# Performance work log

Hardware: AMD Instinct MI355X
Metric: run time of the kernel (lower is better)

## Reference

```python
import jax, jax.numpy as jnp
import numpy as np

N, B, T, H, M, DM, K = 256, 32, 128, 64, 8, 32, 3
IN_DIM = 1
OUT_DIM = 1
DEC_H = H + DM  # 96


def _p(key, shape):
    return jax.random.normal(key, shape, jnp.float32) / np.sqrt(shape[0]).astype(np.float32)


def setup_inputs() -> dict:
    key = jax.random.key(0)
    ks = jax.random.split(key, 10)
    gdi = 2 * K * (IN_DIM + H)      # 390
    ddi = 2 * K * (OUT_DIM + DEC_H)  # 582
    return {
        'x': jax.random.normal(ks[0], (B, T, N, IN_DIM), jnp.float32),
        'Memory': _p(ks[1], (M, DM)),
        'Wq': _p(ks[2], (H, DM)),
        'We1': _p(ks[3], (N, M)),
        'We2': _p(ks[4], (N, M)),
        'enc_gate_w': _p(ks[5], (gdi, 2 * H)), 'enc_gate_b': jnp.zeros((2 * H,), jnp.float32),
        'enc_upd_w': _p(ks[6], (gdi, H)), 'enc_upd_b': jnp.zeros((H,), jnp.float32),
        'dec_gate_w': _p(ks[7], (ddi, 2 * DEC_H)), 'dec_gate_b': jnp.zeros((2 * DEC_H,), jnp.float32),
        'dec_upd_w': _p(ks[8], (ddi, DEC_H)), 'dec_upd_b': jnp.zeros((DEC_H,), jnp.float32),
        'proj_w': _p(ks[9], (DEC_H, OUT_DIM)), 'proj_b': jnp.zeros((OUT_DIM,), jnp.float32),
    }


def _cheb(s):
    # Chebyshev polynomials T_0..T_{K-1} of support s: [I, s, 2 s T_{k-1} - T_{k-2}]
    polys = [jnp.eye(N, dtype=s.dtype), s]
    for _ in range(2, K):
        polys.append(2.0 * s @ polys[-1] - polys[-2])
    return polys


def _scaled_lap(e1, e2, gkey):
    # cosine-similarity graph -> straight-through gumbel hard selection -> scaled Laplacian
    norm = jnp.linalg.norm(e1, axis=1, keepdims=True) @ jnp.linalg.norm(e2, axis=1, keepdims=True).T
    g = (e1 @ e2.T) / (norm + 1e-6)
    g = (g + 1.0) / 2.0
    logits = jnp.stack([g, 1.0 - g], axis=-1)               # (N,N,2)
    y_soft = logits + jax.random.gumbel(gkey, logits.shape, logits.dtype)  # tau=1 (note: source skips softmax)
    y_hard = jax.nn.one_hot(jnp.argmax(y_soft, axis=-1), 2, dtype=logits.dtype)
    adj = (y_hard - jax.lax.stop_gradient(y_soft) + y_soft)[:, :, 0]
    eye = jnp.eye(N, dtype=adj.dtype)
    adj = adj * (1.0 - eye)                                  # zero diagonal
    d = jnp.sum(adj, axis=1)
    L = jnp.diag(d) - adj
    lam = L.max() - L.min()
    return 2.0 * L / lam - eye


def _gconv(x, S, w, b):
    # S: (2K,N,N) stacked cheb supports; x: (B,N,C)
    xg = jnp.einsum('knm,bmc->bnkc', S, x)
    xg = xg.reshape(xg.shape[0], xg.shape[1], -1)            # (B,N,2K*C), support-major like torch cat
    return xg @ w + b


def _cell(x, state, S, gw, gb, uw, ub, hid):
    zr = jax.nn.sigmoid(_gconv(jnp.concatenate([x, state], -1), S, gw, gb))
    z, r = zr[..., :hid], zr[..., hid:]
    hc = jnp.tanh(_gconv(jnp.concatenate([x, z * state], -1), S, uw, ub))
    return r * state + (1.0 - r) * hc


def reference(x, Memory, Wq, We1, We2, enc_gate_w, enc_gate_b, enc_upd_w, enc_upd_b,
              dec_gate_w, dec_gate_b, dec_upd_w, dec_upd_b, proj_w, proj_b):
    k1, k2 = jax.random.split(jax.random.key(42))
    e1, e2 = We1 @ Memory, We2 @ Memory
    S = jnp.stack(_cheb(_scaled_lap(e1, e2, k1)) + _cheb(_scaled_lap(e2, e1, k2)))  # (2K,N,N)

    # --- encoder (1 layer) over time ---
    def enc_step(state, xt):
        h = _cell(xt, state, S, enc_gate_w, enc_gate_b, enc_upd_w, enc_upd_b, H)
        return h, None
    h0 = jnp.zeros((x.shape[0], N, H), x.dtype)
    h_t, _ = jax.lax.scan(enc_step, h0, jnp.swapaxes(x, 0, 1))

    # --- memory attention query ---
    query = h_t @ Wq                                        # (B,N,DM)
    att = jax.nn.softmax(query @ Memory.T, axis=-1)         # (B,N,M)
    value = att @ Memory                                    # (B,N,DM)
    h_de = jnp.concatenate([h_t, value], -1)                # (B,N,DEC_H)

    go0 = jnp.zeros((x.shape[0], N, OUT_DIM), x.dtype)
    def dec_step(carry, _):
        state, go = carry
        h = _cell(go, state, S, dec_gate_w, dec_gate_b, dec_upd_w, dec_upd_b, DEC_H)
        go = h @ proj_w + proj_b
        return (h, go), go
    _, outs = jax.lax.scan(dec_step, (h_de, go0), None, length=T)
    return jnp.swapaxes(outs, 0, 1)                         # (B,T,N,OUT_DIM)
```

## Files before the change

### kernel.cpp

```cpp
#include <hip/hip_runtime.h>
#include <stdint.h>
#include <math.h>

#define NNODE 256
#define BATCH 32
#define TLEN  128
#define ROWS  8192

typedef unsigned short u16;
typedef short bf16x8 __attribute__((ext_vector_type(8)));
typedef float f32x4 __attribute__((ext_vector_type(4)));

__device__ inline u16 f2bf_rn(float v) {
  uint32_t u = __float_as_uint(v);
  u += 0x7fffu + ((u >> 16) & 1u);
  return (u16)(u >> 16);
}
__device__ inline float bf2f(u16 h) { return __uint_as_float(((uint32_t)h) << 16); }
__device__ inline void split2(float v, u16& hi, u16& lo) {
  hi = f2bf_rn(v);
  lo = f2bf_rn(v - bf2f(hi));
}

__device__ inline size_t pk_addr(int c, int b, int n) {
  return ((((size_t)(c >> 4) * 32 + b) * 8 + (n >> 5)) << 9) +
         (((size_t)((c & 15) | (((n >> 3) & 3) << 4))) << 3) + (n & 7);
}

__host__ __device__ inline uint32_t rotl32_(uint32_t v, int d) {
  return (v << d) | (v >> (32 - d));
}
__host__ __device__ inline void tf2x32(uint32_t k0, uint32_t k1, uint32_t x0,
                                       uint32_t x1, uint32_t* o0, uint32_t* o1) {
  uint32_t ks2 = k0 ^ k1 ^ 0x1BD11BDAu;
  x0 += k0; x1 += k1;
  x0 += x1; x1 = rotl32_(x1, 13); x1 ^= x0;
  x0 += x1; x1 = rotl32_(x1, 15); x1 ^= x0;
  x0 += x1; x1 = rotl32_(x1, 26); x1 ^= x0;
  x0 += x1; x1 = rotl32_(x1, 6);  x1 ^= x0;
  x0 += k1; x1 += ks2 + 1u;
  x0 += x1; x1 = rotl32_(x1, 17); x1 ^= x0;
  x0 += x1; x1 = rotl32_(x1, 29); x1 ^= x0;
  x0 += x1; x1 = rotl32_(x1, 16); x1 ^= x0;
  x0 += x1; x1 = rotl32_(x1, 24); x1 ^= x0;
  x0 += ks2; x1 += k0 + 2u;
  x0 += x1; x1 = rotl32_(x1, 13); x1 ^= x0;
  x0 += x1; x1 = rotl32_(x1, 15); x1 ^= x0;
  x0 += x1; x1 = rotl32_(x1, 26); x1 ^= x0;
  x0 += x1; x1 = rotl32_(x1, 6);  x1 ^= x0;
  x0 += k0; x1 += k1 + 3u;
  x0 += x1; x1 = rotl32_(x1, 17); x1 ^= x0;
  x0 += x1; x1 = rotl32_(x1, 29); x1 ^= x0;
  x0 += x1; x1 = rotl32_(x1, 16); x1 ^= x0;
  x0 += x1; x1 = rotl32_(x1, 24); x1 ^= x0;
  x0 += k1; x1 += ks2 + 4u;
  x0 += x1; x1 = rotl32_(x1, 13); x1 ^= x0;
  x0 += x1; x1 = rotl32_(x1, 15); x1 ^= x0;
  x0 += x1; x1 = rotl32_(x1, 26); x1 ^= x0;
  x0 += x1; x1 = rotl32_(x1, 6);  x1 ^= x0;
  x0 += ks2; x1 += k0 + 5u;
  *o0 = x0; *o1 = x1;
}

__device__ inline float gumbel_at(uint32_t k0, uint32_t k1, uint32_t idx) {
  uint32_t o0, o1;
  tf2x32(k0, k1, 0u, idx, &o0, &o1);
  uint32_t b = o0 ^ o1;
  float f = __uint_as_float((b >> 9) | 0x3f800000u) - 1.0f;
  const float tiny = 1.17549435e-38f;
  float u = fmaxf(tiny, f + tiny);
  return -logf(-logf(u));
}

__global__ __launch_bounds__(256) void setup_embed_kernel(
    const float* __restrict__ We1, const float* __restrict__ We2,
    const float* __restrict__ Mem, float* __restrict__ e1, float* __restrict__ e2,
    float* __restrict__ n1, float* __restrict__ n2) {
  int n = threadIdx.x;
  float a[8];
  float s;
  for (int m = 0; m < 8; ++m) a[m] = We1[n * 8 + m];
  s = 0.f;
  for (int j = 0; j < 32; ++j) {
    float v = 0.f;
    for (int m = 0; m < 8; ++m) v = fmaf(a[m], Mem[m * 32 + j], v);
    e1[n * 32 + j] = v;
    s = fmaf(v, v, s);
  }
  n1[n] = sqrtf(s);
  for (int m = 0; m < 8; ++m) a[m] = We2[n * 8 + m];
  s = 0.f;
  for (int j = 0; j < 32; ++j) {
    float v = 0.f;
    for (int m = 0; m < 8; ++m) v = fmaf(a[m], Mem[m * 32 + j], v);
    e2[n * 32 + j] = v;
    s = fmaf(v, v, s);
  }
  n2[n] = sqrtf(s);
}

__global__ void stats_init_kernel(int* stats) {
  stats[0] = 0;
  stats[1] = 0;
  stats[2] = 0x7fffffff;
}

__global__ __launch_bounds__(256) void adj_kernel(
    const float* __restrict__ eA, const float* __restrict__ eB,
    const float* __restrict__ nA, const float* __restrict__ nB,
    uint32_t k0, uint32_t k1, float* __restrict__ adj, float* __restrict__ deg,
    int* __restrict__ stats) {
  int i = blockIdx.x, j = threadIdx.x;
  float dot = 0.f;
  for (int c = 0; c < 32; ++c) dot = fmaf(eA[i * 32 + c], eB[j * 32 + c], dot);
  float g = dot / (nA[i] * nB[j] + 1e-6f);
  g = (g + 1.0f) * 0.5f;
  uint32_t f = ((uint32_t)(i * 256 + j)) * 2u;
  float g0 = gumbel_at(k0, k1, f);
  float g1 = gumbel_at(k0, k1, f + 1u);
  float a = ((g + g0) >= ((1.0f - g) + g1)) ? 1.0f : 0.0f;
  if (i == j) a = 0.0f;
  adj[i * 256 + j] = a;
  __shared__ float red[256];
  red[j] = a;
  __syncthreads();
  for (int s = 128; s > 0; s >>= 1) {
    if (j < s) red[j] += red[j + s];
    __syncthreads();
  }
  if (j == 0) {
    float d = red[0];
    deg[i] = d;
    atomicMax(&stats[0], (int)d);
    atomicMin(&stats[2], (int)d);
    if (d > 0.5f) atomicOr(&stats[1], 1);
  }
}

__global__ __launch_bounds__(256) void lap_kernel(const float* __restrict__ adj,
                                                  const float* __restrict__ deg,
                                                  const int* __restrict__ stats,
                                                  float* __restrict__ S1) {
  int i = blockIdx.x, j = threadIdx.x;
  float lmax = (float)stats[0];
  float lmin = stats[1] ? -1.0f : (float)stats[2];
  float lam = lmax - lmin;
  float L = (i == j) ? deg[i] : -adj[i * 256 + j];
  S1[i * 256 + j] = 2.0f * L / lam - ((i == j) ? 1.0f : 0.0f);
}

__global__ __launch_bounds__(256) void t2_kernel(const float* __restrict__ A,
                                                 float* __restrict__ Cout) {
  __shared__ __align__(16) float sAT[32][68];
  __shared__ __align__(16) float sB[32][68];
  int tid = threadIdx.x;
  int tc = tid & 15, tr = tid >> 4;
  int row0 = blockIdx.y * 64, col0 = blockIdx.x * 64;
  float acc[4][4] = {};
  for (int m0 = 0; m0 < 256; m0 += 32) {
    for (int i = tid; i < 2048; i += 256) {
      int r = i >> 5, c = i & 31;
      sAT[c][r] = A[(size_t)(row0 + r) * 256 + m0 + c];
    }
    for (int i = tid; i < 2048; i += 256) {
      int r = i >> 6, c = i & 63;
      sB[r][c] = A[(size_t)(m0 + r) * 256 + col0 + c];
    }
    __syncthreads();
#pragma unroll
    for (int kk = 0; kk < 32; ++kk) {
      float4 av = *(const float4*)&sAT[kk][tr * 4];
      float4 bv = *(const float4*)&sB[kk][tc * 4];
      float a[4] = {av.x, av.y, av.z, av.w};
      float b[4] = {bv.x, bv.y, bv.z, bv.w};
#pragma unroll
      for (int i = 0; i < 4; ++i)
#pragma unroll
        for (int j = 0; j < 4; ++j) acc[i][j] = fmaf(a[i], b[j], acc[i][j]);
    }
    __syncthreads();
  }
#pragma unroll
  for (int i = 0; i < 4; ++i) {
    int row = row0 + tr * 4 + i;
#pragma unroll
    for (int j = 0; j < 4; ++j) {
      int col = col0 + tc * 4 + j;
      Cout[(size_t)row * 256 + col] = 2.0f * acc[i][j] - ((row == col) ? 1.0f : 0.0f);
    }
  }
}

__global__ void cvt_s_packed(const float* __restrict__ S, u16* __restrict__ Sh,
                             u16* __restrict__ Sl) {
  int idx = blockIdx.x * 256 + threadIdx.x;
  if (idx >= 4 * 65536) return;
  int p = idx >> 16, rem = idx & 65535;
  int n = rem >> 8, m = rem & 255;
  int nt = n >> 4, li = n & 15;
  int mc = m >> 5, g = (m >> 3) & 3, j = m & 7;
  int lane = li | (g << 4);
  size_t a = (((size_t)(p * 16 + nt) * 8 + mc) << 9) + lane * 8 + j;
  u16 h, l;
  split2(S[idx], h, l);
  Sh[a] = h; Sl[a] = l;
}

__global__ void build_wfrag(const float* __restrict__ W, int C, int O, int hid,
                            u16* __restrict__ WfH, u16* __restrict__ WfL,
                            float* __restrict__ w0, float* __restrict__ wlast) {
  int idx = blockIdx.x * 256 + threadIdx.x;
  int nKC = hid / 32;
  if (idx < 5 * hid * O) {
    int kk = idx & 31;
    int rest = idx >> 5;
    int o = rest % O; rest /= O;
    int kc = rest % nKC;
    int p = rest / nKC;
    int korig = (p == 0) ? 0 : (p + (p >= 3 ? 1 : 0));
    int c = kc * 32 + kk;
    float v = 0.f;
    if (c > 0) {
      v = W[(size_t)(korig * C + c) * O + o];
      if (p == 0) v += W[(size_t)(3 * C + c) * O + o];
    }
    int ot = o >> 4, li = o & 15, g = kk >> 3, j = kk & 7;
    int lane = li | (g << 4);
    size_t a = (((size_t)(p * nKC + kc) * (O / 16) + ot) << 9) + lane * 8 + j;
    u16 h, l; split2(v, h, l);
    WfH[a] = h; WfL[a] = l;
  }
  if (idx < 5 * O) {
    int o = idx % O, p = idx / O;
    int korig = (p == 0) ? 0 : (p + (p >= 3 ? 1 : 0));
    float v0 = W[(size_t)(korig * C + 0) * O + o];
    if (p == 0) v0 += W[(size_t)(3 * C + 0) * O + o];
    w0[p * O + o] = v0;
    float vl = W[(size_t)(korig * C + hid) * O + o];
    if (p == 0) vl += W[(size_t)(3 * C + hid) * O + o];
    wlast[p * O + o] = vl;
  }
}

__global__ void zero_kernel(uint4* __restrict__ p, int n4) {
  for (int i = blockIdx.x * blockDim.x + threadIdx.x; i < n4;
       i += gridDim.x * blockDim.x)
    p[i] = make_uint4(0, 0, 0, 0);
}

__global__ void enc_init(const float* __restrict__ x, float* __restrict__ hf,
                         u16* __restrict__ pkh, u16* __restrict__ pkl) {
  int idx = blockIdx.x * 256 + threadIdx.x;
  if (idx >= 65 * ROWS) return;
  int c = idx / ROWS, col = idx % ROWS;
  int b = col >> 8, n = col & 255;
  float v = (c == 0) ? x[(size_t)b * (TLEN * NNODE) + n] : 0.f;
  hf[idx] = v;
  if (c == 0) {
    u16 h, l; split2(v, h, l);
    size_t a = pk_addr(0, b, n);
    pkh[a] = h; pkl[a] = l;
  }
}

__global__ __launch_bounds__(128) void attn2(const float* __restrict__ hEf,
                                             const float* __restrict__ Wq,
                                             const float* __restrict__ Mem,
                                             float* __restrict__ hDf,
                                             u16* __restrict__ pkh,
                                             u16* __restrict__ pkl) {
  int col = blockIdx.x * 128 + threadIdx.x;
  int b = col >> 8, n = col & 255;
  float h[64];
  for (int c = 0; c < 64; ++c) h[c] = hEf[(size_t)(1 + c) * ROWS + col];
  float q[32];
  for (int j = 0; j < 32; ++j) {
    float s = 0.f;
    for (int c = 0; c < 64; ++c) s = fmaf(h[c], Wq[c * 32 + j], s);
    q[j] = s;
  }
  float l[8], mx = -3.402823466e38f;
  for (int m = 0; m < 8; ++m) {
    float s = 0.f;
    for (int j = 0; j < 32; ++j) s = fmaf(q[j], Mem[m * 32 + j], s);
    l[m] = s;
    mx = fmaxf(mx, s);
  }
  float se = 0.f;
  for (int m = 0; m < 8; ++m) { l[m] = expf(l[m] - mx); se += l[m]; }
  float val[32];
  for (int j = 0; j < 32; ++j) {
    float v = 0.f;
    for (int m = 0; m < 8; ++m) v = fmaf(l[m] / se, Mem[m * 32 + j], v);
    val[j] = v;
  }
  for (int c = 0; c < 97; ++c) {
    float v = (c == 0) ? 0.f : ((c <= 64) ? h[c - 1] : val[c - 65]);
    hDf[(size_t)c * ROWS + col] = v;
    u16 hh, ll; split2(v, hh, ll);
    size_t a = pk_addr(c, b, n);
    pkh[a] = hh; pkl[a] = ll;
  }
}

template <int C, int HID, int CPAD, int O, int NKC, int MT1, int MODE>
__global__ __launch_bounds__(512) void fused_step(
    const float* __restrict__ AF,
    const u16* __restrict__ ApkH, const u16* __restrict__ ApkL,
    const u16* __restrict__ SpkH, const u16* __restrict__ SpkL,
    const u16* __restrict__ WpkH, const u16* __restrict__ WpkL,
    const float* __restrict__ w0, const float* __restrict__ wlast,
    const float* __restrict__ bias,
    float* __restrict__ HF, float* __restrict__ outF,
    u16* __restrict__ outPkH, u16* __restrict__ outPkL,
    float* __restrict__ rbuf,
    const float* __restrict__ xsrc, int tnext,
    const float* __restrict__ pw, const float* __restrict__ pb,
    float* __restrict__ outp, int tcur) {
  constexpr int MT2 = O / 16;
  constexpr int MJ2 = (MT2 + 7) / 8;
  constexpr int CH0SLOT = HID + 1;

  __shared__ __align__(16) u16 Gh[2][5][16][CPAD];
  __shared__ __align__(16) u16 Gl[2][5][16][CPAD];
  __shared__ float projL[(MODE == 2) ? 2 : 1][16][(MODE == 2) ? 100 : 1];

  const int tid = threadIdx.x;
  const int wid = tid >> 6, lane = tid & 63;
  const int g = lane >> 4, li = lane & 15;
  const int cg = wid >> 2, pp = wid & 3;
  const int bid0 = (int)blockIdx.x;
  const int bidx = ((bid0 & 7) << 5) | (bid0 >> 3);
  const int col0 = bidx * 32;
  const int b = col0 >> 8;
  const int n0 = (col0 & 255) + cg * 16;
  const int nt = n0 >> 4;

  for (int i = tid; i < 32 * C; i += 512) {
    int c = i >> 5, q = i & 31;
    float v = AF[(size_t)c * ROWS + col0 + q];
    u16 h, l; split2(v, h, l);
    int slot = (c == 0) ? CH0SLOT : c;
    Gh[q >> 4][0][q & 15][slot] = h;
    Gl[q >> 4][0][q & 15][slot] = l;
  }
  if (tid < 32) {
    Gh[tid >> 4][0][tid & 15][0] = 0;
    Gl[tid >> 4][0][tid & 15][0] = 0;
  }

  f32x4 acc1[MT1];
#pragma unroll
  for (int mt = 0; mt < MT1; ++mt) acc1[mt] = (f32x4){0.f, 0.f, 0.f, 0.f};

#pragma unroll 2
  for (int mc = 0; mc < 8; ++mc) {
    size_t sa = (((size_t)(pp * 16 + nt) * 8 + mc) << 9) + lane * 8;
    bf16x8 sbh = *(const bf16x8*)(SpkH + sa);
    bf16x8 sbl = *(const bf16x8*)(SpkL + sa);
#pragma unroll
    for (int mt = 0; mt < MT1; ++mt) {
      size_t aa = (((size_t)(mt * 32 + b) * 8 + mc) << 9) + lane * 8;
      bf16x8 ah = *(const bf16x8*)(ApkH + aa);
      bf16x8 al = *(const bf16x8*)(ApkL + aa);
      acc1[mt] = __builtin_amdgcn_mfma_f32_16x16x32_bf16(ah, sbh, acc1[mt], 0, 0, 0);
      acc1[mt] = __builtin_amdgcn_mfma_f32_16x16x32_bf16(ah, sbl, acc1[mt], 0, 0, 0);
      acc1[mt] = __builtin_amdgcn_mfma_f32_16x16x32_bf16(al, sbh, acc1[mt], 0, 0, 0);
    }
  }

  {
    const int p = pp + 1;
#pragma unroll
    for (int mt = 0; mt < MT1; ++mt) {
      int cq = mt * 16 + 4 * g;
      u16 h4[4], l4[4];
#pragma unroll
      for (int r = 0; r < 4; ++r) split2(acc1[mt][r], h4[r], l4[r]);
      if (cq == 0) {
        Gh[cg][p][li][CH0SLOT] = h4[0];
        Gl[cg][p][li][CH0SLOT] = l4[0];
        h4[0] = 0; l4[0] = 0;
      }
      if (cq + 3 <= HID) {
        uint2 vh, vl;
        vh.x = (uint32_t)h4[0] | ((uint32_t)h4[1] << 16);
        vh.y = (uint32_t)h4[2] | ((uint32_t)h4[3] << 16);
        vl.x = (uint32_t)l4[0] | ((uint32_t)l4[1] << 16);
        vl.y = (uint32_t)l4[2] | ((uint32_t)l4[3] << 16);
        *(uint2*)&Gh[cg][p][li][cq] = vh;
        *(uint2*)&Gl[cg][p][li][cq] = vl;
      } else {
#pragma unroll
        for (int r = 0; r < 4; ++r) {
          int c = cq + r;
          if (c >= 1 && c <= HID) {
            Gh[cg][p][li][c] = h4[r];
            Gl[cg][p][li][c] = l4[r];
          }
        }
      }
    }
  }
  __syncthreads();

  f32x4 acc2[MJ2][2];
#pragma unroll
  for (int j = 0; j < MJ2; ++j)
#pragma unroll
    for (int c2 = 0; c2 < 2; ++c2) acc2[j][c2] = (f32x4){0.f, 0.f, 0.f, 0.f};

#pragma unroll
  for (int p = 0; p < 5; ++p) {
#pragma unroll
    for (int kc = 0; kc < NKC; ++kc) {
      bf16x8 bh[2], bl[2];
#pragma unroll
      for (int c2 = 0; c2 < 2; ++c2) {
        bh[c2] = *(const bf16x8*)&Gh[c2][p][li][kc * 32 + g * 8];
        bl[c2] = *(const bf16x8*)&Gl[c2][p][li][kc * 32 + g * 8];
      }
#pragma unroll
      for (int j = 0; j < MJ2; ++j) {
        const int mt = wid + j * 8;
        if (mt < MT2) {
          size_t wa = (((size_t)(p * NKC + kc) * MT2 + mt) << 9) + lane * 8;
          bf16x8 wh = *(const bf16x8*)(WpkH + wa);
          bf16x8 wl = *(const bf16x8*)(WpkL + wa);
#pragma unroll
          for (int c2 = 0; c2 < 2; ++c2) {
            acc2[j][c2] = __builtin_amdgcn_mfma_f32_16x16x32_bf16(wh, bh[c2], acc2[j][c2], 0, 0, 0);
            acc2[j][c2] = __builtin_amdgcn_mfma_f32_16x16x32_bf16(wh, bl[c2], acc2[j][c2], 0, 0, 0);
            acc2[j][c2] = __builtin_amdgcn_mfma_f32_16x16x32_bf16(wl, bh[c2], acc2[j][c2], 0, 0, 0);
          }
        }
      }
    }
  }

  float ch0v[2][5], clv[2][5];
#pragma unroll
  for (int c2 = 0; c2 < 2; ++c2)
#pragma unroll
    for (int p = 0; p < 5; ++p) {
      ch0v[c2][p] = (p == 0)
          ? AF[col0 + c2 * 16 + li]
          : (bf2f(Gh[c2][p][li][CH0SLOT]) + bf2f(Gl[c2][p][li][CH0SLOT]));
      clv[c2][p] = bf2f(Gh[c2][p][li][HID]) + bf2f(Gl[c2][p][li][HID]);
    }

#pragma unroll
  for (int j = 0; j < MJ2; ++j) {
    const int mt = wid + j * 8;
    if (mt < MT2) {
#pragma unroll
      for (int c2 = 0; c2 < 2; ++c2) {
        const int colx = col0 + c2 * 16 + li;
        const int ncolx = colx & 255;
#pragma unroll
        for (int r = 0; r < 4; ++r) {
          int o = mt * 16 + 4 * g + r;
          float v = acc2[j][c2][r] + bias[o];
#pragma unroll
          for (int p = 0; p < 5; ++p) {
            v = fmaf(w0[p * O + o], ch0v[c2][p], v);
            v = fmaf(wlast[p * O + o], clv[c2][p], v);
          }
          if (MODE == 0) {
            float s = 1.0f / (1.0f + expf(-v));
            if (o < HID) {
              float u = s * HF[(size_t)(1 + o) * ROWS + colx];
              outF[(size_t)(1 + o) * ROWS + colx] = u;
              u16 h_, l_; split2(u, h_, l_);
              size_t a = pk_addr(1 + o, b, ncolx);
              outPkH[a] = h_; outPkL[a] = l_;
            } else {
              rbuf[(size_t)(o - HID) * ROWS + colx] = s;
            }
          } else {
            float hc = tanhf(v);
            float hp = HF[(size_t)(1 + o) * ROWS + colx];
            float rr = rbuf[(size_t)o * ROWS + colx];
            float hn = rr * hp + (1.0f - rr) * hc;
            HF[(size_t)(1 + o) * ROWS + colx] = hn;
            u16 h_, l_; split2(hn, h_, l_);
            size_t a = pk_addr(1 + o, b, ncolx);
            outPkH[a] = h_; outPkL[a] = l_;
            if (MODE == 2) projL[c2][li][o] = hn;
          }
        }
      }
    }
  }

  if (MODE == 0) {
    if (tid < 32) {
      int cc = col0 + tid;
      float x0 = AF[cc];
      outF[cc] = x0;
      u16 h_, l_; split2(x0, h_, l_);
      size_t a = pk_addr(0, b, cc & 255);
      outPkH[a] = h_; outPkL[a] = l_;
    }
  }
  if (MODE == 1) {
    __syncthreads();
    if (tid < 32) {
      int cc = col0 + tid;
      int n = cc & 255;
      float xv = (tnext >= 0)
          ? xsrc[(size_t)b * (TLEN * NNODE) + (size_t)tnext * NNODE + n]
          : HF[cc];
      HF[cc] = xv;
      u16 h_, l_; split2(xv, h_, l_);
      size_t a = pk_addr(0, b, n);
      outPkH[a] = h_; outPkL[a] = l_;
    }
  }
  if (MODE == 2) {
    __syncthreads();
    if (tid < 32) {
      int cc = col0 + tid;
      int n = cc & 255;
      float s = pb[0];
#pragma unroll
      for (int o = 0; o < HID; ++o) s = fmaf(pw[o], projL[tid >> 4][tid & 15][o], s);
      HF[cc] = s;
      u16 h_, l_; split2(s, h_, l_);
      size_t a = pk_addr(0, b, n);
      outPkH[a] = h_; outPkL[a] = l_;
      outp[((size_t)b * TLEN + tcur) * NNODE + n] = s;
    }
  }
}

extern "C" void kernel_launch(void* const* d_in, const int* in_sizes, int n_in,
                              void* d_out, int out_size, void* d_ws, size_t ws_size,
                              hipStream_t stream) {
  (void)in_sizes; (void)n_in; (void)out_size; (void)ws_size;
  const float* x   = (const float*)d_in[0];
  const float* Mem = (const float*)d_in[1];
  const float* Wq  = (const float*)d_in[2];
  const float* We1 = (const float*)d_in[3];
  const float* We2 = (const float*)d_in[4];
  const float* egw = (const float*)d_in[5];
  const float* egb = (const float*)d_in[6];
  const float* euw = (const float*)d_in[7];
  const float* eub = (const float*)d_in[8];
  const float* dgw = (const float*)d_in[9];
  const float* dgb = (const float*)d_in[10];
  const float* duw = (const float*)d_in[11];
  const float* dub = (const float*)d_in[12];
  const float* pw  = (const float*)d_in[13];
  const float* pb  = (const float*)d_in[14];
  float* out = (float*)d_out;

  float* ws = (float*)d_ws;
  size_t off = 0;
  auto allocf = [&](size_t nf) {
    float* p = ws + off;
    off += (nf + 63) & ~(size_t)63;
    return p;
  };
  auto allocu = [&](size_t nu) { return (u16*)allocf((nu + 1) / 2); };

  float* Sf  = allocf(4 * 65536);
  float* e1  = allocf(8192);
  float* e2  = allocf(8192);
  float* n1  = allocf(256);
  float* n2  = allocf(256);
  float* adj = allocf(65536);
  float* deg = allocf(256);
  int* stats = (int*)allocf(64);
  float* rb  = allocf((size_t)96 * ROWS);
  float* hEf = allocf((size_t)65 * ROWS);
  float* uEf = allocf((size_t)65 * ROWS);
  float* hDf = allocf((size_t)97 * ROWS);
  float* uDf = allocf((size_t)97 * ROWS);
  float* w0gE = allocf(5 * 128);
  float* w0uE = allocf(5 * 64);
  float* w0gD = allocf(5 * 192);
  float* w0uD = allocf(5 * 96);
  float* wlgE = allocf(5 * 128);
  float* wluE = allocf(5 * 64);
  float* wlgD = allocf(5 * 192);
  float* wluD = allocf(5 * 96);

  u16* SpkH = allocu((size_t)4 * 65536);
  u16* SpkL = allocu((size_t)4 * 65536);
  u16* WgEh = allocu((size_t)5 * 2 * 8 * 512);
  u16* WgEl = allocu((size_t)5 * 2 * 8 * 512);
  u16* WuEh = allocu((size_t)5 * 2 * 4 * 512);
  u16* WuEl = allocu((size_t)5 * 2 * 4 * 512);
  u16* WgDh = allocu((size_t)5 * 3 * 12 * 512);
  u16* WgDl = allocu((size_t)5 * 3 * 12 * 512);
  u16* WuDh = allocu((size_t)5 * 3 * 6 * 512);
  u16* WuDl = allocu((size_t)5 * 3 * 6 * 512);

  const size_t PKE = (size_t)5 * 32 * 8 * 512;
  const size_t PKD = (size_t)7 * 32 * 8 * 512;
  u16* hEpkH = allocu(PKE);
  u16* hEpkL = allocu(PKE);
  u16* uEpkH = allocu(PKE);
  u16* uEpkL = allocu(PKE);
  u16* hDpkH = allocu(PKD);
  u16* hDpkL = allocu(PKD);
  u16* uDpkH = allocu(PKD);
  u16* uDpkL = allocu(PKD);
  const size_t PKTOT = 4 * PKE + 4 * PKD;

  uint32_t ka0, ka1, kb0, kb1;
  tf2x32(0u, 42u, 0u, 0u, &ka0, &ka1);
  tf2x32(0u, 42u, 0u, 1u, &kb0, &kb1);

  zero_kernel<<<1024, 256, 0, stream>>>((uint4*)hEpkH, (int)(PKTOT / 8));
  setup_embed_kernel<<<1, 256, 0, stream>>>(We1, We2, Mem, e1, e2, n1, n2);
  stats_init_kernel<<<1, 1, 0, stream>>>(stats);
  adj_kernel<<<256, 256, 0, stream>>>(e1, e2, n1, n2, ka0, ka1, adj, deg, stats);
  lap_kernel<<<256, 256, 0, stream>>>(adj, deg, stats, Sf);
  t2_kernel<<<dim3(4, 4), 256, 0, stream>>>(Sf, Sf + 65536);
  stats_init_kernel<<<1, 1, 0, stream>>>(stats);
  adj_kernel<<<256, 256, 0, stream>>>(e2, e1, n2, n1, kb0, kb1, adj, deg, stats);
  lap_kernel<<<256, 256, 0, stream>>>(adj, deg, stats, Sf + 2 * 65536);
  t2_kernel<<<dim3(4, 4), 256, 0, stream>>>(Sf + 2 * 65536, Sf + 3 * 65536);
  cvt_s_packed<<<1024, 256, 0, stream>>>(Sf, SpkH, SpkL);
  build_wfrag<<<(5 * 64 * 128 + 255) / 256, 256, 0, stream>>>(egw, 65, 128, 64, WgEh, WgEl, w0gE, wlgE);
  build_wfrag<<<(5 * 64 * 64 + 255) / 256, 256, 0, stream>>>(euw, 65, 64, 64, WuEh, WuEl, w0uE, wluE);
  build_wfrag<<<(5 * 96 * 192 + 255) / 256, 256, 0, stream>>>(dgw, 97, 192, 96, WgDh, WgDl, w0gD, wlgD);
  build_wfrag<<<(5 * 96 * 96 + 255) / 256, 256, 0, stream>>>(duw, 97, 96, 96, WuDh, WuDl, w0uD, wluD);

  enc_init<<<(65 * ROWS + 255) / 256, 256, 0, stream>>>(x, hEf, hEpkH, hEpkL);
  for (int t = 0; t < TLEN; ++t) {
    fused_step<65, 64, 72, 128, 2, 5, 0><<<256, 512, 0, stream>>>(
        hEf, hEpkH, hEpkL, SpkH, SpkL, WgEh, WgEl, w0gE, wlgE, egb,
        hEf, uEf, uEpkH, uEpkL, rb, nullptr, -1, nullptr, nullptr, nullptr, 0);
    fused_step<65, 64, 72, 64, 2, 5, 1><<<256, 512, 0, stream>>>(
        uEf, uEpkH, uEpkL, SpkH, SpkL, WuEh, WuEl, w0uE, wluE, eub,
        hEf, hEf, hEpkH, hEpkL, rb,
        x, (t + 1 < TLEN) ? (t + 1) : -1, nullptr, nullptr, nullptr, 0);
  }

  attn2<<<64, 128, 0, stream>>>(hEf, Wq, Mem, hDf, hDpkH, hDpkL);

  for (int t = 0; t < TLEN; ++t) {
    fused_step<97, 96, 104, 192, 3, 7, 0><<<256, 512, 0, stream>>>(
        hDf, hDpkH, hDpkL, SpkH, SpkL, WgDh, WgDl, w0gD, wlgD, dgb,
        hDf, uDf, uDpkH, uDpkL, rb, nullptr, -1, nullptr, nullptr, nullptr, 0);
    fused_step<97, 96, 104, 96, 3, 7, 2><<<256, 512, 0, stream>>>(
        uDf, uDpkH, uDpkL, SpkH, SpkL, WuDh, WuDl, w0uD, wluD, dub,
        hDf, hDf, hDpkH, hDpkL, rb,
        nullptr, -1, pw, pb, out, t);
  }
}
```

Baseline: 9.302 ms.

## Double fused_step block to 1024 threads and split MFMA tiles across waves

Each fused GRU step kernel now runs 16 waves instead of 8. In the graph-propagation stage, each wave handles half of the row tiles, selected by a new `half` index. In the weight-GEMM stage, each wave owns a single output tile instead of looping over several. The goal is to cut per-block serial MFMA latency on a grid of only 256 blocks with a long chain of dependent launches. The trade-offs: the encoder update step leaves most waves idle in stage two, and `__launch_bounds__(1024, 4)` may squeeze the register budget and cause spills.

```diff
diff --git a/kernel.cpp b/kernel.cpp
--- a/kernel.cpp
+++ b/kernel.cpp
@@ -304,7 +304,7 @@
 }
 
 template <int C, int HID, int CPAD, int O, int NKC, int MT1, int MODE>
-__global__ __launch_bounds__(512) void fused_step(
+__global__ __launch_bounds__(1024, 4) void fused_step(
     const float* __restrict__ AF,
     const u16* __restrict__ ApkH, const u16* __restrict__ ApkL,
     const u16* __restrict__ SpkH, const u16* __restrict__ SpkL,
@@ -318,7 +318,7 @@
     const float* __restrict__ pw, const float* __restrict__ pb,
     float* __restrict__ outp, int tcur) {
   constexpr int MT2 = O / 16;
-  constexpr int MJ2 = (MT2 + 7) / 8;
+  constexpr int MT1A = (MT1 + 1) / 2;
   constexpr int CH0SLOT = HID + 1;
 
   __shared__ __align__(16) u16 Gh[2][5][16][CPAD];
@@ -328,7 +328,7 @@
   const int tid = threadIdx.x;
   const int wid = tid >> 6, lane = tid & 63;
   const int g = lane >> 4, li = lane & 15;
-  const int cg = wid >> 2, pp = wid & 3;
+  const int cg = wid >> 3, pp = wid & 3, half = (wid >> 2) & 1;
   const int bid0 = (int)blockIdx.x;
   const int bidx = ((bid0 & 7) << 5) | (bid0 >> 3);
   const int col0 = bidx * 32;
@@ -336,7 +336,7 @@
   const int n0 = (col0 & 255) + cg * 16;
   const int nt = n0 >> 4;
 
-  for (int i = tid; i < 32 * C; i += 512) {
+  for (int i = tid; i < 32 * C; i += 1024) {
     int c = i >> 5, q = i & 31;
     float v = AF[(size_t)c * ROWS + col0 + q];
     u16 h, l; split2(v, h, l);
@@ -349,9 +349,9 @@
     Gl[tid >> 4][0][tid & 15][0] = 0;
   }
 
-  f32x4 acc1[MT1];
-#pragma unroll
-  for (int mt = 0; mt < MT1; ++mt) acc1[mt] = (f32x4){0.f, 0.f, 0.f, 0.f};
+  f32x4 acc1[MT1A];
+#pragma unroll
+  for (int i = 0; i < MT1A; ++i) acc1[i] = (f32x4){0.f, 0.f, 0.f, 0.f};
 
 #pragma unroll 2
   for (int mc = 0; mc < 8; ++mc) {
@@ -359,44 +359,50 @@
     bf16x8 sbh = *(const bf16x8*)(SpkH + sa);
     bf16x8 sbl = *(const bf16x8*)(SpkL + sa);
 #pragma unroll
-    for (int mt = 0; mt < MT1; ++mt) {
-      size_t aa = (((size_t)(mt * 32 + b) * 8 + mc) << 9) + lane * 8;
-      bf16x8 ah = *(const bf16x8*)(ApkH + aa);
-      bf16x8 al = *(const bf16x8*)(ApkL + aa);
-      acc1[mt] = __builtin_amdgcn_mfma_f32_16x16x32_bf16(ah, sbh, acc1[mt], 0, 0, 0);
-      acc1[mt] = __builtin_amdgcn_mfma_f32_16x16x32_bf16(ah, sbl, acc1[mt], 0, 0, 0);
-      acc1[mt] = __builtin_amdgcn_mfma_f32_16x16x32_bf16(al, sbh, acc1[mt], 0, 0, 0);
+    for (int i = 0; i < MT1A; ++i) {
+      const int mt = half * MT1A + i;
+      if (mt < MT1) {
+        size_t aa = (((size_t)(mt * 32 + b) * 8 + mc) << 9) + lane * 8;
+        bf16x8 ah = *(const bf16x8*)(ApkH + aa);
+        bf16x8 al = *(const bf16x8*)(ApkL + aa);
+        acc1[i] = __builtin_amdgcn_mfma_f32_16x16x32_bf16(ah, sbh, acc1[i], 0, 0, 0);
+        acc1[i] = __builtin_amdgcn_mfma_f32_16x16x32_bf16(ah, sbl, acc1[i], 0, 0, 0);
+        acc1[i] = __builtin_amdgcn_mfma_f32_16x16x32_bf16(al, sbh, acc1[i], 0, 0, 0);
+      }
     }
   }
 
   {
     const int p = pp + 1;
 #pragma unroll
-    for (int mt = 0; mt < MT1; ++mt) {
-      int cq = mt * 16 + 4 * g;
-      u16 h4[4], l4[4];
-#pragma unroll
-      for (int r = 0; r < 4; ++r) split2(acc1[mt][r], h4[r], l4[r]);
-      if (cq == 0) {
-        Gh[cg][p][li][CH0SLOT] = h4[0];
-        Gl[cg][p][li][CH0SLOT] = l4[0];
-        h4[0] = 0; l4[0] = 0;
-      }
-      if (cq + 3 <= HID) {
-        uint2 vh, vl;
-        vh.x = (uint32_t)h4[0] | ((uint32_t)h4[1] << 16);
-        vh.y = (uint32_t)h4[2] | ((uint32_t)h4[3] << 16);
-        vl.x = (uint32_t)l4[0] | ((uint32_t)l4[1] << 16);
-        vl.y = (uint32_t)l4[2] | ((uint32_t)l4[3] << 16);
-        *(uint2*)&Gh[cg][p][li][cq] = vh;
-        *(uint2*)&Gl[cg][p][li][cq] = vl;
-      } else {
-#pragma unroll
-        for (int r = 0; r < 4; ++r) {
-          int c = cq + r;
-          if (c >= 1 && c <= HID) {
-            Gh[cg][p][li][c] = h4[r];
-            Gl[cg][p][li][c] = l4[r];
+    for (int i = 0; i < MT1A; ++i) {
+      const int mt = half * MT1A + i;
+      if (mt < MT1) {
+        int cq = mt * 16 + 4 * g;
+        u16 h4[4], l4[4];
+#pragma unroll
+        for (int r = 0; r < 4; ++r) split2(acc1[i][r], h4[r], l4[r]);
+        if (cq == 0) {
+          Gh[cg][p][li][CH0SLOT] = h4[0];
+          Gl[cg][p][li][CH0SLOT] = l4[0];
+          h4[0] = 0; l4[0] = 0;
+        }
+        if (cq + 3 <= HID) {
+          uint2 vh, vl;
+          vh.x = (uint32_t)h4[0] | ((uint32_t)h4[1] << 16);
+          vh.y = (uint32_t)h4[2] | ((uint32_t)h4[3] << 16);
+          vl.x = (uint32_t)l4[0] | ((uint32_t)l4[1] << 16);
+          vl.y = (uint32_t)l4[2] | ((uint32_t)l4[3] << 16);
+          *(uint2*)&Gh[cg][p][li][cq] = vh;
+          *(uint2*)&Gl[cg][p][li][cq] = vl;
+        } else {
+#pragma unroll
+          for (int r = 0; r < 4; ++r) {
+            int c = cq + r;
+            if (c >= 1 && c <= HID) {
+              Gh[cg][p][li][c] = h4[r];
+              Gl[cg][p][li][c] = l4[r];
+            }
           }
         }
       }
@@ -404,35 +410,29 @@
   }
   __syncthreads();
 
-  f32x4 acc2[MJ2][2];
-#pragma unroll
-  for (int j = 0; j < MJ2; ++j)
-#pragma unroll
-    for (int c2 = 0; c2 < 2; ++c2) acc2[j][c2] = (f32x4){0.f, 0.f, 0.f, 0.f};
-
-#pragma unroll
-  for (int p = 0; p < 5; ++p) {
-#pragma unroll
-    for (int kc = 0; kc < NKC; ++kc) {
-      bf16x8 bh[2], bl[2];
-#pragma unroll
-      for (int c2 = 0; c2 < 2; ++c2) {
-        bh[c2] = *(const bf16x8*)&Gh[c2][p][li][kc * 32 + g * 8];
-        bl[c2] = *(const bf16x8*)&Gl[c2][p][li][kc * 32 + g * 8];
-      }
-#pragma unroll
-      for (int j = 0; j < MJ2; ++j) {
-        const int mt = wid + j * 8;
-        if (mt < MT2) {
-          size_t wa = (((size_t)(p * NKC + kc) * MT2 + mt) << 9) + lane * 8;
-          bf16x8 wh = *(const bf16x8*)(WpkH + wa);
-          bf16x8 wl = *(const bf16x8*)(WpkL + wa);
-#pragma unroll
-          for (int c2 = 0; c2 < 2; ++c2) {
-            acc2[j][c2] = __builtin_amdgcn_mfma_f32_16x16x32_bf16(wh, bh[c2], acc2[j][c2], 0, 0, 0);
-            acc2[j][c2] = __builtin_amdgcn_mfma_f32_16x16x32_bf16(wh, bl[c2], acc2[j][c2], 0, 0, 0);
-            acc2[j][c2] = __builtin_amdgcn_mfma_f32_16x16x32_bf16(wl, bh[c2], acc2[j][c2], 0, 0, 0);
-          }
+  const int mt2 = wid;
+  f32x4 acc2[2];
+  acc2[0] = (f32x4){0.f, 0.f, 0.f, 0.f};
+  acc2[1] = (f32x4){0.f, 0.f, 0.f, 0.f};
+  if (mt2 < MT2) {
+#pragma unroll
+    for (int p = 0; p < 5; ++p) {
+#pragma unroll
+      for (int kc = 0; kc < NKC; ++kc) {
+        bf16x8 bh[2], bl[2];
+#pragma unroll
+        for (int c2 = 0; c2 < 2; ++c2) {
+          bh[c2] = *(const bf16x8*)&Gh[c2][p][li][kc * 32 + g * 8];
+          bl[c2] = *(const bf16x8*)&Gl[c2][p][li][kc * 32 + g * 8];
+        }
+        size_t wa = (((size_t)(p * NKC + kc) * MT2 + mt2) << 9) + lane * 8;
+        bf16x8 wh = *(const bf16x8*)(WpkH + wa);
+        bf16x8 wl = *(const bf16x8*)(WpkL + wa);
+#pragma unroll
+        for (int c2 = 0; c2 < 2; ++c2) {
+          acc2[c2] = __builtin_amdgcn_mfma_f32_16x16x32_bf16(wh, bh[c2], acc2[c2], 0, 0, 0);
+          acc2[c2] = __builtin_amdgcn_mfma_f32_16x16x32_bf16(wh, bl[c2], acc2[c2], 0, 0, 0);
+          acc2[c2] = __builtin_amdgcn_mfma_f32_16x16x32_bf16(wl, bh[c2], acc2[c2], 0, 0, 0);
         }
       }
     }
@@ -449,45 +449,41 @@
       clv[c2][p] = bf2f(Gh[c2][p][li][HID]) + bf2f(Gl[c2][p][li][HID]);
     }
 
-#pragma unroll
-  for (int j = 0; j < MJ2; ++j) {
-    const int mt = wid + j * 8;
-    if (mt < MT2) {
-#pragma unroll
-      for (int c2 = 0; c2 < 2; ++c2) {
-        const int colx = col0 + c2 * 16 + li;
-        const int ncolx = colx & 255;
-#pragma unroll
-        for (int r = 0; r < 4; ++r) {
-          int o = mt * 16 + 4 * g + r;
-          float v = acc2[j][c2][r] + bias[o];
-#pragma unroll
-          for (int p = 0; p < 5; ++p) {
-            v = fmaf(w0[p * O + o], ch0v[c2][p], v);
-            v = fmaf(wlast[p * O + o], clv[c2][p], v);
-          }
-          if (MODE == 0) {
-            float s = 1.0f / (1.0f + expf(-v));
-            if (o < HID) {
-              float u = s * HF[(size_t)(1 + o) * ROWS + colx];
-              outF[(size_t)(1 + o) * ROWS + colx] = u;
-              u16 h_, l_; split2(u, h_, l_);
-              size_t a = pk_addr(1 + o, b, ncolx);
-              outPkH[a] = h_; outPkL[a] = l_;
-            } else {
-              rbuf[(size_t)(o - HID) * ROWS + colx] = s;
-            }
-          } else {
-            float hc = tanhf(v);
-            float hp = HF[(size_t)(1 + o) * ROWS + colx];
-            float rr = rbuf[(size_t)o * ROWS + colx];
-            float hn = rr * hp + (1.0f - rr) * hc;
-            HF[(size_t)(1 + o) * ROWS + colx] = hn;
-            u16 h_, l_; split2(hn, h_, l_);
+  if (mt2 < MT2) {
+#pragma unroll
+    for (int c2 = 0; c2 < 2; ++c2) {
+      const int colx = col0 + c2 * 16 + li;
+      const int ncolx = colx & 255;
+#pragma unroll
+      for (int r = 0; r < 4; ++r) {
+        int o = mt2 * 16 + 4 * g + r;
+        float v = acc2[c2][r] + bias[o];
+#pragma unroll
+        for (int p = 0; p < 5; ++p) {
+          v = fmaf(w0[p * O + o], ch0v[c2][p], v);
+          v = fmaf(wlast[p * O + o], clv[c2][p], v);
+        }
+        if (MODE == 0) {
+          float s = 1.0f / (1.0f + expf(-v));
+          if (o < HID) {
+            float u = s * HF[(size_t)(1 + o) * ROWS + colx];
+            outF[(size_t)(1 + o) * ROWS + colx] = u;
+            u16 h_, l_; split2(u, h_, l_);
             size_t a = pk_addr(1 + o, b, ncolx);
             outPkH[a] = h_; outPkL[a] = l_;
-            if (MODE == 2) projL[c2][li][o] = hn;
+          } else {
+            rbuf[(size_t)(o - HID) * ROWS + colx] = s;
           }
+        } else {
+          float hc = tanhf(v);
+          float hp = HF[(size_t)(1 + o) * ROWS + colx];
+          float rr = rbuf[(size_t)o * ROWS + colx];
+          float hn = rr * hp + (1.0f - rr) * hc;
+          HF[(size_t)(1 + o) * ROWS + colx] = hn;
+          u16 h_, l_; split2(hn, h_, l_);
+          size_t a = pk_addr(1 + o, b, ncolx);
+          outPkH[a] = h_; outPkL[a] = l_;
+          if (MODE == 2) projL[c2][li][o] = hn;
         }
       }
     }
@@ -631,10 +627,10 @@
 
   enc_init<<<(65 * ROWS + 255) / 256, 256, 0, stream>>>(x, hEf, hEpkH, hEpkL);
   for (int t = 0; t < TLEN; ++t) {
-    fused_step<65, 64, 72, 128, 2, 5, 0><<<256, 512, 0, stream>>>(
+    fused_step<65, 64, 72, 128, 2, 5, 0><<<256, 1024, 0, stream>>>(
         hEf, hEpkH, hEpkL, SpkH, SpkL, WgEh, WgEl, w0gE, wlgE, egb,
         hEf, uEf, uEpkH, uEpkL, rb, nullptr, -1, nullptr, nullptr, nullptr, 0);
-    fused_step<65, 64, 72, 64, 2, 5, 1><<<256, 512, 0, stream>>>(
+    fused_step<65, 64, 72, 64, 2, 5, 1><<<256, 1024, 0, stream>>>(
         uEf, uEpkH, uEpkL, SpkH, SpkL, WuEh, WuEl, w0uE, wluE, eub,
         hEf, hEf, hEpkH, hEpkL, rb,
         x, (t + 1 < TLEN) ? (t + 1) : -1, nullptr, nullptr, nullptr, 0);
@@ -643,10 +639,10 @@
   attn2<<<64, 128, 0, stream>>>(hEf, Wq, Mem, hDf, hDpkH, hDpkL);
 
   for (int t = 0; t < TLEN; ++t) {
-    fused_step<97, 96, 104, 192, 3, 7, 0><<<256, 512, 0, stream>>>(
+    fused_step<97, 96, 104, 192, 3, 7, 0><<<256, 1024, 0, stream>>>(
         hDf, hDpkH, hDpkL, SpkH, SpkL, WgDh, WgDl, w0gD, wlgD, dgb,
         hDf, uDf, uDpkH, uDpkL, rb, nullptr, -1, nullptr, nullptr, nullptr, 0);
-    fused_step<97, 96, 104, 96, 3, 7, 2><<<256, 512, 0, stream>>>(
+    fused_step<97, 96, 104, 96, 3, 7, 2><<<256, 1024, 0, stream>>>(
         uDf, uDpkH, uDpkL, SpkH, SpkL, WuDh, WuDl, w0uD, wluD, dub,
         hDf, hDf, hDpkH, hDpkL, rb,
         nullptr, -1, pw, pb, out, t);
```

Result: faster. 8.907 ms (-4.2%).
